# Kernel tuning notes

Hardware: AMD Instinct MI355X
Metric: run time of the kernel (lower is better)

## Reference

```python
import jax, jax.numpy as jnp
import numpy as np

D_MODEL = 768
STATE_N = 16
BATCH = 8
SEQ = 2048


def setup_inputs() -> dict:
    key = jax.random.key(0)
    ks = jax.random.split(key, 12)
    d, n = D_MODEL, STATE_N
    s = 0.02
    inp = {
        "x": jax.random.normal(ks[0], (BATCH, SEQ, d), dtype=jnp.float32),
        # A_log init as in module: log(arange(1..N)) repeated over d_model
        "A_log": jnp.log(jnp.tile(jnp.arange(1, n + 1, dtype=jnp.float32)[None, :], (d, 1))),
        "D_param": jnp.ones((d,), dtype=jnp.float32),
        "B_proj_w": jax.random.normal(ks[1], (n, d), dtype=jnp.float32) * s,
        "C_proj_w": jax.random.normal(ks[2], (n, d), dtype=jnp.float32) * s,
        "delta_w": jax.random.normal(ks[3], (d, d), dtype=jnp.float32) * s,
        "delta_b": jax.random.normal(ks[4], (d,), dtype=jnp.float32) * s,
        "in_w": jax.random.normal(ks[5], (2 * d, d), dtype=jnp.float32) * s,
        "in_b": jax.random.normal(ks[6], (2 * d,), dtype=jnp.float32) * s,
        "out_w": jax.random.normal(ks[7], (d, d), dtype=jnp.float32) * s,
        "out_b": jax.random.normal(ks[8], (d,), dtype=jnp.float32) * s,
        "conv_w": jax.random.normal(ks[9], (d, 1, 3), dtype=jnp.float32) * s,  # depthwise [D,1,K]
        "conv_b": jax.random.normal(ks[10], (d,), dtype=jnp.float32) * s,
    }
    return inp


def _forward(x, A_log, D_param, B_proj_w, C_proj_w, delta_w, delta_b,
             in_w, in_b, out_w, out_b, conv_w, conv_b):
    A = -jnp.exp(A_log)  # [D, N]
    xz = jnp.einsum("bld,ed->ble", x, in_w) + in_b  # [B, L, 2D]
    x_in, z = jnp.split(xz, 2, axis=-1)
    # depthwise conv1d, padding=1, groups=D (cross-correlation, same as torch)
    x_c = jax.lax.conv_general_dilated(
        jnp.transpose(x_in, (0, 2, 1)), conv_w,
        window_strides=(1,), padding=((1, 1),),
        feature_group_count=x.shape[-1],
        dimension_numbers=("NCH", "OIH", "NCH"))
    x_conv = jnp.transpose(x_c, (0, 2, 1)) + conv_b  # [B, L, D]
    x_conv = jax.nn.silu(x_conv)
    delta = jax.nn.softplus(jnp.einsum("bld,ed->ble", x_conv, delta_w) + delta_b)  # [B,L,D]
    B_sel = jnp.einsum("bld,nd->bln", x_conv, B_proj_w)  # [B, L, N]
    C_sel = jnp.einsum("bld,nd->bln", x_conv, C_proj_w)  # [B, L, N]

    Bsz, L, D = x.shape
    N = A.shape[1]

    def step(h, t_in):
        dt, b_t, c_t, x_t = t_in  # [B,D], [B,N], [B,N], [B,D]
        A_bar = jnp.exp(dt[:, :, None] * A[None, :, :])           # [B,D,N]
        h = A_bar * h + (dt[:, :, None] * b_t[:, None, :]) * x_t[:, :, None]
        y_t = jnp.sum(h * c_t[:, None, :], axis=-1)               # [B,D]
        return h, y_t

    xs = (jnp.transpose(delta, (1, 0, 2)), jnp.transpose(B_sel, (1, 0, 2)),
          jnp.transpose(C_sel, (1, 0, 2)), jnp.transpose(x_conv, (1, 0, 2)))
    h0 = jnp.zeros((Bsz, D, N), dtype=x.dtype)
    _, ys = jax.lax.scan(step, h0, xs)
    y = jnp.transpose(ys, (1, 0, 2))  # [B, L, D]

    y = y + x_conv * D_param[None, None, :]
    y = y * jax.nn.silu(z)
    return jnp.einsum("bld,ed->ble", y, out_w) + out_b


def reference(x, A_log, D_param, B_proj_w, C_proj_w, delta_w, delta_b,
              in_w, in_b, out_w, out_b, conv_w, conv_b):
    return _forward(x, A_log, D_param, B_proj_w, C_proj_w, delta_w, delta_b,
                    in_w, in_b, out_w, out_b, conv_w, conv_b)
```

## Files before the change

kernel.cpp:

```cpp
#include <hip/hip_runtime.h>
#include <hip/hip_bf16.h>

#define D_MODEL 768
#define SEQL    2048
#define BATCH   8
#define NSTATE  16
#define NCHUNK  32
#define TCHUNK  64

typedef __attribute__((ext_vector_type(8))) short short8;
typedef __attribute__((ext_vector_type(4))) float f32x4;

typedef const __attribute__((address_space(1))) unsigned int gas1_t;
typedef __attribute__((address_space(3))) unsigned int las3_t;

__device__ __forceinline__ void gload_lds16(const void* g, void* l) {
  __builtin_amdgcn_global_load_lds((gas1_t*)g, (las3_t*)l, 16, 0, 0);
}

__global__ __launch_bounds__(256) void prep_all(
    const float* __restrict__ x, const float* __restrict__ in_w,
    const float* __restrict__ delta_w, const float* __restrict__ Bp,
    const float* __restrict__ Cp, const float* __restrict__ out_w,
    const float* __restrict__ A_log,
    __hip_bfloat16* __restrict__ xb, __hip_bfloat16* __restrict__ w_in,
    __hip_bfloat16* __restrict__ w_dbc, __hip_bfloat16* __restrict__ w_out,
    float* __restrict__ A2) {
  int i = blockIdx.x * 256 + threadIdx.x;
  if (i < 3145728) {
    int j = i * 4;
    float4 v = *(const float4*)(x + j);
    xb[j + 0] = __float2bfloat16(v.x);
    xb[j + 1] = __float2bfloat16(v.y);
    xb[j + 2] = __float2bfloat16(v.z);
    xb[j + 3] = __float2bfloat16(v.w);
    return;
  }
  i -= 3145728;
  if (i < 1536 * 768) { w_in[i] = __float2bfloat16(in_w[i]); return; }
  i -= 1536 * 768;
  if (i < 896 * 768) {
    int row = i / 768, col = i - row * 768;
    float v;
    if (row < 768)      v = delta_w[row * 768 + col];
    else if (row < 784) v = Bp[(row - 768) * 768 + col];
    else if (row < 800) v = Cp[(row - 784) * 768 + col];
    else                v = 0.f;
    w_dbc[i] = __float2bfloat16(v);
    return;
  }
  i -= 896 * 768;
  if (i < 768 * 768) { w_out[i] = __float2bfloat16(out_w[i]); return; }
  i -= 768 * 768;
  A2[i] = -expf(A_log[i]) * 1.44269504088896f;
}

template <int MODE>
__global__ __launch_bounds__(256, 2) void gemm128(
    const __hip_bfloat16* __restrict__ Amat, const __hip_bfloat16* __restrict__ Bw,
    const float* __restrict__ bias, void* __restrict__ out0,
    void* __restrict__ out1, void* __restrict__ out2,
    const int K, const int gxn) {
  __shared__ char lds[65536];
  const int tid  = threadIdx.x;
  const int lane = tid & 63, wave = tid >> 6;
  const int wr = wave >> 1, wc = wave & 1;

  const int nwg = gridDim.x, id = blockIdx.x;
  const int swz = (id & 7) * (nwg >> 3) + (id >> 3);
  const int tm = swz / gxn, tn = swz - tm * gxn;
  const int rowA0 = tm * 128, rowB0 = tn * 128;

  const int srow = tid >> 3;
  const int scol = ((((tid & 7) << 4) ^ ((srow & 7) << 4)) >> 1);
  const __hip_bfloat16* gA = Amat + (size_t)(rowA0 + srow) * K + scol;
  const __hip_bfloat16* gB = Bw   + (size_t)(rowB0 + srow) * K + scol;
  const int ldst = tid << 4;

  const int frow = lane & 15, fq = lane >> 4;
  const int fswz = (frow & 7) << 4;
  const int pc0 = (fq << 4) ^ fswz;
  const int pc1 = (64 | (fq << 4)) ^ fswz;
  const int aro = (wr * 64 + frow) << 7;
  const int bro = (wc * 64 + frow) << 7;

  f32x4 acc[4][4];
#pragma unroll
  for (int m = 0; m < 4; ++m)
#pragma unroll
    for (int n = 0; n < 4; ++n) acc[m][n] = (f32x4){0.f, 0.f, 0.f, 0.f};

#define SA(buf) (lds + ((buf) << 15))
#define SB(buf) (lds + ((buf) << 15) + 16384)
#define STAGE(buf, kt)                                                          \
  {                                                                             \
    const __hip_bfloat16* spA = gA + (size_t)(kt) * 64;                         \
    const __hip_bfloat16* spB = gB + (size_t)(kt) * 64;                         \
    char* dA = SA(buf) + ldst;                                                  \
    char* dB = SB(buf) + ldst;                                                  \
    _Pragma("unroll") for (int ss = 0; ss < 4; ++ss)                            \
        gload_lds16(spA + (size_t)(ss * 32) * K, dA + ss * 4096);               \
    _Pragma("unroll") for (int ss = 0; ss < 4; ++ss)                            \
        gload_lds16(spB + (size_t)(ss * 32) * K, dB + ss * 4096);               \
  }

  short8 a[4][2], b[2][2];
#define LOADA(sAp)                                                              \
  {                                                                             \
    _Pragma("unroll") for (int m = 0; m < 4; ++m) {                             \
      const char* p = (sAp) + aro + ((m * 16) << 7);                            \
      a[m][0] = *(const short8*)(p + pc0);                                      \
      a[m][1] = *(const short8*)(p + pc1);                                      \
    }                                                                           \
  }
#define LOADB(sBp, nh)                                                          \
  {                                                                             \
    _Pragma("unroll") for (int n = 0; n < 2; ++n) {                             \
      const char* p = (sBp) + bro + ((((nh)*2 + n) * 16) << 7);                 \
      b[n][0] = *(const short8*)(p + pc0);                                      \
      b[n][1] = *(const short8*)(p + pc1);                                      \
    }                                                                           \
  }
#define MMA(nh)                                                                 \
  {                                                                             \
    __builtin_amdgcn_s_setprio(1);                                              \
    _Pragma("unroll") for (int m = 0; m < 4; ++m)                               \
    _Pragma("unroll") for (int n = 0; n < 2; ++n)                               \
    _Pragma("unroll") for (int ks = 0; ks < 2; ++ks)                            \
        acc[m][(nh)*2 + n] = __builtin_amdgcn_mfma_f32_16x16x32_bf16(           \
            a[m][ks], b[n][ks], acc[m][(nh)*2 + n], 0, 0, 0);                   \
    __builtin_amdgcn_s_setprio(0);                                              \
  }

  STAGE(0, 0);
  asm volatile("s_waitcnt vmcnt(0)" ::: "memory");
  __builtin_amdgcn_s_barrier();

  const int NT = K >> 6;
  for (int kt = 0; kt < NT; ++kt) {
    const int cur = kt & 1, nxt = cur ^ 1;
    const bool st = (kt + 1 < NT);
    LOADA(SA(cur));
    LOADB(SB(cur), 0);
    if (st) STAGE(nxt, kt + 1);
    __builtin_amdgcn_s_barrier();
    MMA(0);
    __builtin_amdgcn_s_barrier();
    LOADB(SB(cur), 1);
    __builtin_amdgcn_s_barrier();
    MMA(1);
    asm volatile("s_waitcnt vmcnt(0)" ::: "memory");
    __builtin_amdgcn_s_barrier();
  }

#pragma unroll
  for (int m = 0; m < 4; ++m) {
    const int grow0 = rowA0 + wr * 64 + m * 16 + fq * 4;
#pragma unroll
    for (int n = 0; n < 4; ++n) {
      const int gcol = rowB0 + wc * 64 + n * 16 + frow;
#pragma unroll
      for (int i = 0; i < 4; ++i) {
        const size_t grow = grow0 + i;
        float v = acc[m][n][i];
        if (MODE == 0) {
          v += bias[gcol];
          if (gcol < 768)
            ((__hip_bfloat16*)out0)[grow * 768 + gcol] = __float2bfloat16(v);
          else
            ((__hip_bfloat16*)out1)[grow * 768 + gcol - 768] = __float2bfloat16(v);
        } else if (MODE == 1) {
          if (gcol < 768) {
            v += bias[gcol];
            float sp = (v > 20.f) ? v : log1pf(expf(v));
            ((__hip_bfloat16*)out0)[grow * 768 + gcol] = __float2bfloat16(sp);
          } else if (gcol < 784) {
            ((float*)out1)[grow * 16 + (gcol - 768)] = v;
          } else if (gcol < 800) {
            ((float*)out2)[grow * 16 + (gcol - 784)] = v;
          }
        } else {
          ((float*)out0)[grow * 768 + gcol] = v + bias[gcol];
        }
      }
    }
  }
#undef SA
#undef SB
#undef STAGE
#undef LOADA
#undef LOADB
#undef MMA
}

__global__ __launch_bounds__(256) void conv_silu(
    const __hip_bfloat16* __restrict__ xin, const float* __restrict__ conv_w,
    const float* __restrict__ conv_b, __hip_bfloat16* __restrict__ xc) {
  const int idx = blockIdx.x * 256 + threadIdx.x;
  const int d = idx % 768;
  const int t = (idx / 768) % SEQL;
  const float w0 = conv_w[d * 3], w1 = conv_w[d * 3 + 1], w2 = conv_w[d * 3 + 2];
  float acc = conv_b[d];
  float xm = (t > 0)        ? __bfloat162float(xin[idx - 768]) : 0.f;
  float x0 = __bfloat162float(xin[idx]);
  float xp = (t < SEQL - 1) ? __bfloat162float(xin[idx + 768]) : 0.f;
  acc += w0 * xm + w1 * x0 + w2 * xp;
  const float sig = 1.f / (1.f + __expf(-acc));
  xc[idx] = __float2bfloat16(acc * sig);
}

__global__ __launch_bounds__(256) void scan_pass1(
    const __hip_bfloat16* __restrict__ delta, const __hip_bfloat16* __restrict__ xconv,
    const float* __restrict__ Bsel, const float* __restrict__ A2,
    float* __restrict__ sumdt, float* __restrict__ Sbuf) {
  const int d = blockIdx.x * 256 + threadIdx.x;
  const int b = blockIdx.y, c = blockIdx.z;
  __shared__ float sB[TCHUNK * 16];
  ((float4*)sB)[threadIdx.x] =
      ((const float4*)(Bsel + ((size_t)b * SEQL + c * TCHUNK) * 16))[threadIdx.x];
  __syncthreads();

  float a2[16];
#pragma unroll
  for (int n = 0; n < 16; ++n) a2[n] = A2[d * 16 + n];
  float h[16] = {};
  float sdt = 0.f;
  const size_t base = ((size_t)b * SEQL + c * TCHUNK) * 768 + d;
  for (int t = 0; t < TCHUNK; ++t) {
    const float dt = __bfloat162float(delta[base + (size_t)t * 768]);
    const float x = __bfloat162float(xconv[base + (size_t)t * 768]);
    sdt += dt;
    const float dtx = dt * x;
    const float* Br = &sB[t * 16];
#pragma unroll
    for (int n = 0; n < 16; ++n) {
      const float a = exp2f(dt * a2[n]);
      h[n] = fmaf(a, h[n], dtx * Br[n]);
    }
  }
  sumdt[((size_t)b * NCHUNK + c) * 768 + d] = sdt;
#pragma unroll
  for (int n = 0; n < 16; ++n)
    Sbuf[(((size_t)b * NCHUNK + c) * 16 + n) * 768 + d] = h[n];
}

__global__ __launch_bounds__(256) void scan_carry(
    const float* __restrict__ sumdt, const float* __restrict__ Sbuf,
    const float* __restrict__ A2, float* __restrict__ Hin) {
  const int idx = blockIdx.x * 256 + threadIdx.x;
  const int d = idx % 768;
  const int n = (idx / 768) & 15;
  const int b = idx / (768 * 16);
  const float a2 = A2[d * 16 + n];
  float h = 0.f;
  for (int c = 0; c < NCHUNK; ++c) {
    const size_t hb = (((size_t)(b * NCHUNK + c)) * 16 + n) * 768 + d;
    Hin[hb] = h;
    const float sd = sumdt[(b * NCHUNK + c) * 768 + d];
    h = fmaf(exp2f(sd * a2), h, Sbuf[hb]);
  }
}

__global__ __launch_bounds__(256) void scan_pass3(
    const __hip_bfloat16* __restrict__ delta, const __hip_bfloat16* __restrict__ xconv,
    const __hip_bfloat16* __restrict__ zb, const float* __restrict__ Bsel,
    const float* __restrict__ Csel, const float* __restrict__ A2,
    const float* __restrict__ Hin, const float* __restrict__ Dp,
    __hip_bfloat16* __restrict__ yg) {
  const int d = blockIdx.x * 256 + threadIdx.x;
  const int b = blockIdx.y, c = blockIdx.z;
  __shared__ float sB[TCHUNK * 16], sC[TCHUNK * 16];
  {
    const size_t off = ((size_t)b * SEQL + c * TCHUNK) * 16;
    ((float4*)sB)[threadIdx.x] = ((const float4*)(Bsel + off))[threadIdx.x];
    ((float4*)sC)[threadIdx.x] = ((const float4*)(Csel + off))[threadIdx.x];
  }
  __syncthreads();

  float a2[16];
#pragma unroll
  for (int n = 0; n < 16; ++n) a2[n] = A2[d * 16 + n];
  float h[16];
  {
    const size_t hb = ((size_t)b * NCHUNK + c) * 16 * 768 + d;
#pragma unroll
    for (int n = 0; n < 16; ++n) h[n] = Hin[hb + (size_t)n * 768];
  }
  const float Dpd = Dp[d];
  const size_t base = ((size_t)b * SEQL + c * TCHUNK) * 768 + d;
  for (int t = 0; t < TCHUNK; ++t) {
    const float dt = __bfloat162float(delta[base + (size_t)t * 768]);
    const float x = __bfloat162float(xconv[base + (size_t)t * 768]);
    const float dtx = dt * x;
    const float* Br = &sB[t * 16];
    const float* Cr = &sC[t * 16];
    float y = 0.f;
#pragma unroll
    for (int n = 0; n < 16; ++n) {
      const float a = exp2f(dt * a2[n]);
      h[n] = fmaf(a, h[n], dtx * Br[n]);
      y = fmaf(h[n], Cr[n], y);
    }
    const float z = __bfloat162float(zb[base + (size_t)t * 768]);
    const float sig = 1.f / (1.f + __expf(-z));
    const float out = (y + x * Dpd) * (z * sig);
    yg[base + (size_t)t * 768] = __float2bfloat16(out);
  }
}

extern "C" void kernel_launch(void* const* d_in, const int* in_sizes, int n_in,
                              void* d_out, int out_size, void* d_ws, size_t ws_size,
                              hipStream_t stream) {
  const float* x       = (const float*)d_in[0];
  const float* A_log   = (const float*)d_in[1];
  const float* D_param = (const float*)d_in[2];
  const float* B_proj  = (const float*)d_in[3];
  const float* C_proj  = (const float*)d_in[4];
  const float* delta_w = (const float*)d_in[5];
  const float* delta_b = (const float*)d_in[6];
  const float* in_w    = (const float*)d_in[7];
  const float* in_b    = (const float*)d_in[8];
  const float* out_w   = (const float*)d_in[9];
  const float* out_b   = (const float*)d_in[10];
  const float* conv_w  = (const float*)d_in[11];
  const float* conv_b  = (const float*)d_in[12];

  char* ws = (char*)d_ws;
  __hip_bfloat16* xb       = (__hip_bfloat16*)(ws + 0);
  __hip_bfloat16* w_in_b   = (__hip_bfloat16*)(ws + 25165824);
  __hip_bfloat16* w_dbc_b  = (__hip_bfloat16*)(ws + 27525120);
  __hip_bfloat16* w_out_b  = (__hip_bfloat16*)(ws + 28901376);
  float*          A2       = (float*)(ws + 30081024);
  __hip_bfloat16* xin_b    = (__hip_bfloat16*)(ws + 30130176);
  __hip_bfloat16* z_b      = (__hip_bfloat16*)(ws + 55296000);
  __hip_bfloat16* xconv_b  = (__hip_bfloat16*)(ws + 80461824);
  __hip_bfloat16* delta_bf = (__hip_bfloat16*)(ws + 105627648);
  float*          Bsel     = (float*)(ws + 130793472);
  float*          Csel     = (float*)(ws + 131842048);
  float*          sumdt    = (float*)(ws + 132890624);
  float*          Sbuf     = (float*)(ws + 133677056);
  float*          Hin      = (float*)(ws + 146259968);
  __hip_bfloat16* yg       = xb;

  const int BLD = BATCH * SEQL * D_MODEL;

  prep_all<<<21936, 256, 0, stream>>>(x, in_w, delta_w, B_proj, C_proj, out_w, A_log,
                                      xb, w_in_b, w_dbc_b, w_out_b, A2);
  gemm128<0><<<1536, 256, 0, stream>>>(xb, w_in_b, in_b, xin_b, z_b, nullptr, 768, 12);
  conv_silu<<<BLD / 256, 256, 0, stream>>>(xin_b, conv_w, conv_b, xconv_b);
  gemm128<1><<<896, 256, 0, stream>>>(xconv_b, w_dbc_b, delta_b, delta_bf, Bsel, Csel, 768, 7);
  scan_pass1<<<dim3(3, BATCH, NCHUNK), 256, 0, stream>>>(delta_bf, xconv_b, Bsel, A2, sumdt, Sbuf);
  scan_carry<<<384, 256, 0, stream>>>(sumdt, Sbuf, A2, Hin);
  scan_pass3<<<dim3(3, BATCH, NCHUNK), 256, 0, stream>>>(delta_bf, xconv_b, z_b, Bsel, Csel, A2,
                                                         Hin, D_param, yg);
  gemm128<2><<<768, 256, 0, stream>>>(yg, w_out_b, out_b, (float*)d_out, nullptr, nullptr, 768, 6);
}
```

Measured before the change: 383.9 us.

## Replace 128x128 GEMM with 256x256 tiled 8-wave kernel and interleaved staging

The GEMM kernel moves from 128x128 tiles with 4 waves to 256x256 tiles with 8 waves and 128KB of LDS. Global-to-LDS staging is split into quarter-tile pieces and interleaved with the four MMA phases using partial vmcnt waits. K is fixed at compile time. The delta/B/C weight matrix is padded to 1024 rows and the workspace offsets are shifted to match. The larger tiles should raise data reuse per byte loaded, but they cut the grid to 192-384 blocks, which risks poor CU utilisation. 128KB of LDS per block also likely keeps occupancy to one block per CU.

```diff
diff --git a/kernel.cpp b/kernel.cpp
--- a/kernel.cpp
+++ b/kernel.cpp
@@ -39,7 +39,7 @@
   i -= 3145728;
   if (i < 1536 * 768) { w_in[i] = __float2bfloat16(in_w[i]); return; }
   i -= 1536 * 768;
-  if (i < 896 * 768) {
+  if (i < 1024 * 768) {
     int row = i / 768, col = i - row * 768;
     float v;
     if (row < 768)      v = delta_w[row * 768 + col];
@@ -49,32 +49,32 @@
     w_dbc[i] = __float2bfloat16(v);
     return;
   }
-  i -= 896 * 768;
+  i -= 1024 * 768;
   if (i < 768 * 768) { w_out[i] = __float2bfloat16(out_w[i]); return; }
   i -= 768 * 768;
   A2[i] = -expf(A_log[i]) * 1.44269504088896f;
 }
 
 template <int MODE>
-__global__ __launch_bounds__(256, 2) void gemm128(
+__global__ __launch_bounds__(512, 2) void gemm256(
     const __hip_bfloat16* __restrict__ Amat, const __hip_bfloat16* __restrict__ Bw,
     const float* __restrict__ bias, void* __restrict__ out0,
-    void* __restrict__ out1, void* __restrict__ out2,
-    const int K, const int gxn) {
-  __shared__ char lds[65536];
+    void* __restrict__ out1, void* __restrict__ out2, const int gxn) {
+  constexpr int K = 768;
+  __shared__ char lds[131072];
   const int tid  = threadIdx.x;
   const int lane = tid & 63, wave = tid >> 6;
-  const int wr = wave >> 1, wc = wave & 1;
+  const int wr = wave >> 2, wc = wave & 3;
 
   const int nwg = gridDim.x, id = blockIdx.x;
   const int swz = (id & 7) * (nwg >> 3) + (id >> 3);
   const int tm = swz / gxn, tn = swz - tm * gxn;
-  const int rowA0 = tm * 128, rowB0 = tn * 128;
-
-  const int srow = tid >> 3;
-  const int scol = ((((tid & 7) << 4) ^ ((srow & 7) << 4)) >> 1);
-  const __hip_bfloat16* gA = Amat + (size_t)(rowA0 + srow) * K + scol;
-  const __hip_bfloat16* gB = Bw   + (size_t)(rowB0 + srow) * K + scol;
+  const int rowA0 = tm * 256, rowB0 = tn * 256;
+
+  const int srow0 = tid >> 3;
+  const int scol  = (((tid & 7) ^ (srow0 & 7)) << 3);
+  const __hip_bfloat16* gA = Amat + (size_t)(rowA0 + srow0) * K + scol;
+  const __hip_bfloat16* gB = Bw   + (size_t)(rowB0 + srow0) * K + scol;
   const int ldst = tid << 4;
 
   const int frow = lane & 15, fq = lane >> 4;
@@ -82,115 +82,155 @@
   const int pc0 = (fq << 4) ^ fswz;
   const int pc1 = (64 | (fq << 4)) ^ fswz;
   const int aro = (wr * 64 + frow) << 7;
-  const int bro = (wc * 64 + frow) << 7;
-
-  f32x4 acc[4][4];
-#pragma unroll
-  for (int m = 0; m < 4; ++m)
-#pragma unroll
-    for (int n = 0; n < 4; ++n) acc[m][n] = (f32x4){0.f, 0.f, 0.f, 0.f};
-
-#define SA(buf) (lds + ((buf) << 15))
-#define SB(buf) (lds + ((buf) << 15) + 16384)
-#define STAGE(buf, kt)                                                          \
-  {                                                                             \
-    const __hip_bfloat16* spA = gA + (size_t)(kt) * 64;                         \
-    const __hip_bfloat16* spB = gB + (size_t)(kt) * 64;                         \
-    char* dA = SA(buf) + ldst;                                                  \
-    char* dB = SB(buf) + ldst;                                                  \
-    _Pragma("unroll") for (int ss = 0; ss < 4; ++ss)                            \
-        gload_lds16(spA + (size_t)(ss * 32) * K, dA + ss * 4096);               \
-    _Pragma("unroll") for (int ss = 0; ss < 4; ++ss)                            \
-        gload_lds16(spB + (size_t)(ss * 32) * K, dB + ss * 4096);               \
+  const int bro = (wc * 32 + frow) << 7;
+
+  f32x4 acc[2][2][4][2];
+#pragma unroll
+  for (int mh = 0; mh < 2; ++mh)
+#pragma unroll
+    for (int nh = 0; nh < 2; ++nh)
+#pragma unroll
+      for (int m = 0; m < 4; ++m)
+#pragma unroll
+        for (int n = 0; n < 2; ++n) acc[mh][nh][m][n] = (f32x4){0.f, 0.f, 0.f, 0.f};
+
+#define STAGE_AH(d, h, kt)                                                      \
+  {                                                                             \
+    const __hip_bfloat16* s0 = gA + (size_t)((h)*128) * K + (kt)*64;            \
+    char* d0 = lds + ((d) << 16) + ((h) << 14) + ldst;                          \
+    gload_lds16(s0, d0);                                                        \
+    gload_lds16(s0 + (size_t)64 * K, d0 + 8192);                                \
+  }
+#define STAGE_BH(d, h, kt)                                                      \
+  {                                                                             \
+    const __hip_bfloat16* s0 = gB + (size_t)((h)*128) * K + (kt)*64;            \
+    char* d0 = lds + ((d) << 16) + 32768 + ((h) << 14) + ldst;                  \
+    gload_lds16(s0, d0);                                                        \
+    gload_lds16(s0 + (size_t)64 * K, d0 + 8192);                                \
   }
 
   short8 a[4][2], b[2][2];
-#define LOADA(sAp)                                                              \
-  {                                                                             \
+#define LOADA(d, mh)                                                            \
+  {                                                                             \
+    const char* base = lds + ((d) << 16) + ((mh) << 14) + aro;                  \
     _Pragma("unroll") for (int m = 0; m < 4; ++m) {                             \
-      const char* p = (sAp) + aro + ((m * 16) << 7);                            \
+      const char* p = base + ((m * 16) << 7);                                   \
       a[m][0] = *(const short8*)(p + pc0);                                      \
       a[m][1] = *(const short8*)(p + pc1);                                      \
     }                                                                           \
   }
-#define LOADB(sBp, nh)                                                          \
-  {                                                                             \
+#define LOADB(d, nh)                                                            \
+  {                                                                             \
+    const char* base = lds + ((d) << 16) + 32768 + ((nh) << 14) + bro;          \
     _Pragma("unroll") for (int n = 0; n < 2; ++n) {                             \
-      const char* p = (sBp) + bro + ((((nh)*2 + n) * 16) << 7);                 \
+      const char* p = base + ((n * 16) << 7);                                   \
       b[n][0] = *(const short8*)(p + pc0);                                      \
       b[n][1] = *(const short8*)(p + pc1);                                      \
     }                                                                           \
   }
-#define MMA(nh)                                                                 \
+#define MMA(mh, nh)                                                             \
   {                                                                             \
     __builtin_amdgcn_s_setprio(1);                                              \
     _Pragma("unroll") for (int m = 0; m < 4; ++m)                               \
     _Pragma("unroll") for (int n = 0; n < 2; ++n)                               \
     _Pragma("unroll") for (int ks = 0; ks < 2; ++ks)                            \
-        acc[m][(nh)*2 + n] = __builtin_amdgcn_mfma_f32_16x16x32_bf16(           \
-            a[m][ks], b[n][ks], acc[m][(nh)*2 + n], 0, 0, 0);                   \
+        acc[mh][nh][m][n] = __builtin_amdgcn_mfma_f32_16x16x32_bf16(            \
+            a[m][ks], b[n][ks], acc[mh][nh][m][n], 0, 0, 0);                    \
     __builtin_amdgcn_s_setprio(0);                                              \
   }
-
-  STAGE(0, 0);
-  asm volatile("s_waitcnt vmcnt(0)" ::: "memory");
-  __builtin_amdgcn_s_barrier();
-
-  const int NT = K >> 6;
-  for (int kt = 0; kt < NT; ++kt) {
+#define VMW(n) asm volatile("s_waitcnt vmcnt(" #n ")" ::: "memory")
+
+  STAGE_AH(0, 0, 0);
+  STAGE_BH(0, 0, 0);
+  STAGE_BH(0, 1, 0);
+  STAGE_AH(0, 1, 0);
+
+  constexpr int NT = K / 64;
+  for (int kt = 0; kt < NT - 1; ++kt) {
     const int cur = kt & 1, nxt = cur ^ 1;
-    const bool st = (kt + 1 < NT);
-    LOADA(SA(cur));
-    LOADB(SB(cur), 0);
-    if (st) STAGE(nxt, kt + 1);
-    __builtin_amdgcn_s_barrier();
-    MMA(0);
-    __builtin_amdgcn_s_barrier();
-    LOADB(SB(cur), 1);
-    __builtin_amdgcn_s_barrier();
-    MMA(1);
-    asm volatile("s_waitcnt vmcnt(0)" ::: "memory");
-    __builtin_amdgcn_s_barrier();
-  }
-
-#pragma unroll
-  for (int m = 0; m < 4; ++m) {
-    const int grow0 = rowA0 + wr * 64 + m * 16 + fq * 4;
-#pragma unroll
-    for (int n = 0; n < 4; ++n) {
-      const int gcol = rowB0 + wc * 64 + n * 16 + frow;
-#pragma unroll
-      for (int i = 0; i < 4; ++i) {
-        const size_t grow = grow0 + i;
-        float v = acc[m][n][i];
-        if (MODE == 0) {
-          v += bias[gcol];
-          if (gcol < 768)
-            ((__hip_bfloat16*)out0)[grow * 768 + gcol] = __float2bfloat16(v);
-          else
-            ((__hip_bfloat16*)out1)[grow * 768 + gcol - 768] = __float2bfloat16(v);
-        } else if (MODE == 1) {
-          if (gcol < 768) {
-            v += bias[gcol];
-            float sp = (v > 20.f) ? v : log1pf(expf(v));
-            ((__hip_bfloat16*)out0)[grow * 768 + gcol] = __float2bfloat16(sp);
-          } else if (gcol < 784) {
-            ((float*)out1)[grow * 16 + (gcol - 768)] = v;
-          } else if (gcol < 800) {
-            ((float*)out2)[grow * 16 + (gcol - 784)] = v;
+    VMW(4);
+    __builtin_amdgcn_s_barrier();
+    LOADA(cur, 0);
+    LOADB(cur, 0);
+    STAGE_AH(nxt, 0, kt + 1);
+    MMA(0, 0);
+    VMW(4);
+    __builtin_amdgcn_s_barrier();
+    LOADB(cur, 1);
+    STAGE_BH(nxt, 0, kt + 1);
+    MMA(0, 1);
+    VMW(4);
+    __builtin_amdgcn_s_barrier();
+    LOADA(cur, 1);
+    STAGE_BH(nxt, 1, kt + 1);
+    MMA(1, 1);
+    __builtin_amdgcn_s_barrier();
+    LOADB(cur, 0);
+    STAGE_AH(nxt, 1, kt + 1);
+    MMA(1, 0);
+  }
+  {
+    const int cur = (NT - 1) & 1;
+    VMW(4);
+    __builtin_amdgcn_s_barrier();
+    LOADA(cur, 0);
+    LOADB(cur, 0);
+    MMA(0, 0);
+    VMW(2);
+    __builtin_amdgcn_s_barrier();
+    LOADB(cur, 1);
+    MMA(0, 1);
+    VMW(0);
+    __builtin_amdgcn_s_barrier();
+    LOADA(cur, 1);
+    MMA(1, 1);
+    __builtin_amdgcn_s_barrier();
+    LOADB(cur, 0);
+    MMA(1, 0);
+  }
+
+#pragma unroll
+  for (int mh = 0; mh < 2; ++mh)
+#pragma unroll
+    for (int nh = 0; nh < 2; ++nh)
+#pragma unroll
+      for (int m = 0; m < 4; ++m) {
+        const int grow0 = rowA0 + mh * 128 + wr * 64 + m * 16 + fq * 4;
+#pragma unroll
+        for (int n = 0; n < 2; ++n) {
+          const int gcol = rowB0 + nh * 128 + wc * 32 + n * 16 + frow;
+#pragma unroll
+          for (int i = 0; i < 4; ++i) {
+            const size_t grow = grow0 + i;
+            float v = acc[mh][nh][m][n][i];
+            if (MODE == 0) {
+              v += bias[gcol];
+              if (gcol < 768)
+                ((__hip_bfloat16*)out0)[grow * 768 + gcol] = __float2bfloat16(v);
+              else
+                ((__hip_bfloat16*)out1)[grow * 768 + gcol - 768] = __float2bfloat16(v);
+            } else if (MODE == 1) {
+              if (gcol < 768) {
+                v += bias[gcol];
+                float sp = (v > 20.f) ? v : log1pf(expf(v));
+                ((__hip_bfloat16*)out0)[grow * 768 + gcol] = __float2bfloat16(sp);
+              } else if (gcol < 784) {
+                ((float*)out1)[grow * 16 + (gcol - 768)] = v;
+              } else if (gcol < 800) {
+                ((float*)out2)[grow * 16 + (gcol - 784)] = v;
+              }
+            } else {
+              ((float*)out0)[grow * 768 + gcol] = v + bias[gcol];
+            }
           }
-        } else {
-          ((float*)out0)[grow * 768 + gcol] = v + bias[gcol];
         }
       }
-    }
-  }
-#undef SA
-#undef SB
-#undef STAGE
+#undef STAGE_AH
+#undef STAGE_BH
 #undef LOADA
 #undef LOADB
 #undef MMA
+#undef VMW
 }
 
 __global__ __launch_bounds__(256) void conv_silu(
@@ -329,29 +369,29 @@
   __hip_bfloat16* xb       = (__hip_bfloat16*)(ws + 0);
   __hip_bfloat16* w_in_b   = (__hip_bfloat16*)(ws + 25165824);
   __hip_bfloat16* w_dbc_b  = (__hip_bfloat16*)(ws + 27525120);
-  __hip_bfloat16* w_out_b  = (__hip_bfloat16*)(ws + 28901376);
-  float*          A2       = (float*)(ws + 30081024);
-  __hip_bfloat16* xin_b    = (__hip_bfloat16*)(ws + 30130176);
-  __hip_bfloat16* z_b      = (__hip_bfloat16*)(ws + 55296000);
-  __hip_bfloat16* xconv_b  = (__hip_bfloat16*)(ws + 80461824);
-  __hip_bfloat16* delta_bf = (__hip_bfloat16*)(ws + 105627648);
-  float*          Bsel     = (float*)(ws + 130793472);
-  float*          Csel     = (float*)(ws + 131842048);
-  float*          sumdt    = (float*)(ws + 132890624);
-  float*          Sbuf     = (float*)(ws + 133677056);
-  float*          Hin      = (float*)(ws + 146259968);
+  __hip_bfloat16* w_out_b  = (__hip_bfloat16*)(ws + 29097984);
+  float*          A2       = (float*)(ws + 30277632);
+  __hip_bfloat16* xin_b    = (__hip_bfloat16*)(ws + 30326784);
+  __hip_bfloat16* z_b      = (__hip_bfloat16*)(ws + 55492608);
+  __hip_bfloat16* xconv_b  = (__hip_bfloat16*)(ws + 80658432);
+  __hip_bfloat16* delta_bf = (__hip_bfloat16*)(ws + 105824256);
+  float*          Bsel     = (float*)(ws + 130990080);
+  float*          Csel     = (float*)(ws + 132038656);
+  float*          sumdt    = (float*)(ws + 133087232);
+  float*          Sbuf     = (float*)(ws + 133873664);
+  float*          Hin      = (float*)(ws + 146456576);
   __hip_bfloat16* yg       = xb;
 
   const int BLD = BATCH * SEQL * D_MODEL;
 
-  prep_all<<<21936, 256, 0, stream>>>(x, in_w, delta_w, B_proj, C_proj, out_w, A_log,
+  prep_all<<<22320, 256, 0, stream>>>(x, in_w, delta_w, B_proj, C_proj, out_w, A_log,
                                       xb, w_in_b, w_dbc_b, w_out_b, A2);
-  gemm128<0><<<1536, 256, 0, stream>>>(xb, w_in_b, in_b, xin_b, z_b, nullptr, 768, 12);
+  gemm256<0><<<384, 512, 0, stream>>>(xb, w_in_b, in_b, xin_b, z_b, nullptr, 6);
   conv_silu<<<BLD / 256, 256, 0, stream>>>(xin_b, conv_w, conv_b, xconv_b);
-  gemm128<1><<<896, 256, 0, stream>>>(xconv_b, w_dbc_b, delta_b, delta_bf, Bsel, Csel, 768, 7);
+  gemm256<1><<<256, 512, 0, stream>>>(xconv_b, w_dbc_b, delta_b, delta_bf, Bsel, Csel, 4);
   scan_pass1<<<dim3(3, BATCH, NCHUNK), 256, 0, stream>>>(delta_bf, xconv_b, Bsel, A2, sumdt, Sbuf);
   scan_carry<<<384, 256, 0, stream>>>(sumdt, Sbuf, A2, Hin);
   scan_pass3<<<dim3(3, BATCH, NCHUNK), 256, 0, stream>>>(delta_bf, xconv_b, z_b, Bsel, Csel, A2,
                                                          Hin, D_param, yg);
-  gemm128<2><<<768, 256, 0, stream>>>(yg, w_out_b, out_b, (float*)d_out, nullptr, nullptr, 768, 6);
-}
+  gemm256<2><<<192, 512, 0, stream>>>(yg, w_out_b, out_b, (float*)d_out, nullptr, nullptr, 3);
+}
```

New measurement: 363.8 us. -5.2%, faster.

## Triple-buffer GEMM with BK=32 pipeline and vectorize conv_silu by 8

Applied to the files above, without the earlier changes.

The GEMM moves from a double-buffered BK=64 loop with four barriers per step to a triple-buffered BK=32 loop that prefetches two stages ahead, with one barrier per step. K is now a compile-time constant, and a smaller LDS footprint allows three workgroups per CU. The depthwise conv+SiLU now handles 8 channels per thread using 16-byte loads and stores, and the scan kernels use a cheaper bit-shift bf16-to-float conversion. The trade-off is twice as many loop iterations, each with fewer MFMAs to hide latency, plus higher register pressure from the 3-wave occupancy bound.

```diff
diff --git a/kernel.cpp b/kernel.cpp
--- a/kernel.cpp
+++ b/kernel.cpp
@@ -16,6 +16,14 @@
 
 __device__ __forceinline__ void gload_lds16(const void* g, void* l) {
   __builtin_amdgcn_global_load_lds((gas1_t*)g, (las3_t*)l, 16, 0, 0);
+}
+
+__device__ __forceinline__ float b2f(short s) {
+  return __uint_as_float(((unsigned)(unsigned short)s) << 16);
+}
+__device__ __forceinline__ short f2b(float f) {
+  __hip_bfloat16 h = __float2bfloat16(f);
+  return *reinterpret_cast<short*>(&h);
 }
 
 __global__ __launch_bounds__(256) void prep_all(
@@ -56,12 +64,13 @@
 }
 
 template <int MODE>
-__global__ __launch_bounds__(256, 2) void gemm128(
+__global__ __launch_bounds__(256, 3) void gemm128tb(
     const __hip_bfloat16* __restrict__ Amat, const __hip_bfloat16* __restrict__ Bw,
     const float* __restrict__ bias, void* __restrict__ out0,
-    void* __restrict__ out1, void* __restrict__ out2,
-    const int K, const int gxn) {
-  __shared__ char lds[65536];
+    void* __restrict__ out1, void* __restrict__ out2, const int gxn) {
+  constexpr int K  = 768;
+  constexpr int KT = 24;
+  __shared__ char lds[49152];
   const int tid  = threadIdx.x;
   const int lane = tid & 63, wave = tid >> 6;
   const int wr = wave >> 1, wc = wave & 1;
@@ -71,18 +80,16 @@
   const int tm = swz / gxn, tn = swz - tm * gxn;
   const int rowA0 = tm * 128, rowB0 = tn * 128;
 
-  const int srow = tid >> 3;
-  const int scol = ((((tid & 7) << 4) ^ ((srow & 7) << 4)) >> 1);
+  const int srow = tid >> 2;
+  const int scol = (((tid & 3) ^ ((srow >> 1) & 3)) << 3);
   const __hip_bfloat16* gA = Amat + (size_t)(rowA0 + srow) * K + scol;
   const __hip_bfloat16* gB = Bw   + (size_t)(rowB0 + srow) * K + scol;
   const int ldst = tid << 4;
 
   const int frow = lane & 15, fq = lane >> 4;
-  const int fswz = (frow & 7) << 4;
-  const int pc0 = (fq << 4) ^ fswz;
-  const int pc1 = (64 | (fq << 4)) ^ fswz;
-  const int aro = (wr * 64 + frow) << 7;
-  const int bro = (wc * 64 + frow) << 7;
+  const int pc = (fq << 4) ^ (((frow >> 1) & 3) << 4);
+  const int aoff = ((wr * 64 + frow) << 6) + pc;
+  const int boff = ((wc * 64 + frow) << 6) + pc;
 
   f32x4 acc[4][4];
 #pragma unroll
@@ -90,67 +97,49 @@
 #pragma unroll
     for (int n = 0; n < 4; ++n) acc[m][n] = (f32x4){0.f, 0.f, 0.f, 0.f};
 
-#define SA(buf) (lds + ((buf) << 15))
-#define SB(buf) (lds + ((buf) << 15) + 16384)
 #define STAGE(buf, kt)                                                          \
   {                                                                             \
-    const __hip_bfloat16* spA = gA + (size_t)(kt) * 64;                         \
-    const __hip_bfloat16* spB = gB + (size_t)(kt) * 64;                         \
-    char* dA = SA(buf) + ldst;                                                  \
-    char* dB = SB(buf) + ldst;                                                  \
-    _Pragma("unroll") for (int ss = 0; ss < 4; ++ss)                            \
-        gload_lds16(spA + (size_t)(ss * 32) * K, dA + ss * 4096);               \
-    _Pragma("unroll") for (int ss = 0; ss < 4; ++ss)                            \
-        gload_lds16(spB + (size_t)(ss * 32) * K, dB + ss * 4096);               \
-  }
-
-  short8 a[4][2], b[2][2];
-#define LOADA(sAp)                                                              \
-  {                                                                             \
-    _Pragma("unroll") for (int m = 0; m < 4; ++m) {                             \
-      const char* p = (sAp) + aro + ((m * 16) << 7);                            \
-      a[m][0] = *(const short8*)(p + pc0);                                      \
-      a[m][1] = *(const short8*)(p + pc1);                                      \
-    }                                                                           \
-  }
-#define LOADB(sBp, nh)                                                          \
-  {                                                                             \
-    _Pragma("unroll") for (int n = 0; n < 2; ++n) {                             \
-      const char* p = (sBp) + bro + ((((nh)*2 + n) * 16) << 7);                 \
-      b[n][0] = *(const short8*)(p + pc0);                                      \
-      b[n][1] = *(const short8*)(p + pc1);                                      \
-    }                                                                           \
-  }
-#define MMA(nh)                                                                 \
-  {                                                                             \
-    __builtin_amdgcn_s_setprio(1);                                              \
-    _Pragma("unroll") for (int m = 0; m < 4; ++m)                               \
-    _Pragma("unroll") for (int n = 0; n < 2; ++n)                               \
-    _Pragma("unroll") for (int ks = 0; ks < 2; ++ks)                            \
-        acc[m][(nh)*2 + n] = __builtin_amdgcn_mfma_f32_16x16x32_bf16(           \
-            a[m][ks], b[n][ks], acc[m][(nh)*2 + n], 0, 0, 0);                   \
-    __builtin_amdgcn_s_setprio(0);                                              \
-  }
+    const __hip_bfloat16* sA = gA + (kt) * 32;                                  \
+    const __hip_bfloat16* sB = gB + (kt) * 32;                                  \
+    char* dA = lds + (buf) * 16384 + ldst;                                      \
+    char* dB = dA + 8192;                                                       \
+    gload_lds16(sA, dA);                                                        \
+    gload_lds16(sA + (size_t)64 * K, dA + 4096);                                \
+    gload_lds16(sB, dB);                                                        \
+    gload_lds16(sB + (size_t)64 * K, dB + 4096);                                \
+  }
+#define VMW(n) asm volatile("s_waitcnt vmcnt(" #n ")" ::: "memory")
+#define BAR    __builtin_amdgcn_s_barrier()
 
   STAGE(0, 0);
-  asm volatile("s_waitcnt vmcnt(0)" ::: "memory");
-  __builtin_amdgcn_s_barrier();
-
-  const int NT = K >> 6;
-  for (int kt = 0; kt < NT; ++kt) {
-    const int cur = kt & 1, nxt = cur ^ 1;
-    const bool st = (kt + 1 < NT);
-    LOADA(SA(cur));
-    LOADB(SB(cur), 0);
-    if (st) STAGE(nxt, kt + 1);
-    __builtin_amdgcn_s_barrier();
-    MMA(0);
-    __builtin_amdgcn_s_barrier();
-    LOADB(SB(cur), 1);
-    __builtin_amdgcn_s_barrier();
-    MMA(1);
-    asm volatile("s_waitcnt vmcnt(0)" ::: "memory");
-    __builtin_amdgcn_s_barrier();
+  STAGE(1, 1);
+  VMW(4);
+  BAR;
+
+  int bc = 0;
+  for (int kt = 0; kt < KT; ++kt) {
+    short8 a[4], b[4];
+    const char* ba = lds + bc * 16384;
+#pragma unroll
+    for (int m = 0; m < 4; ++m) a[m] = *(const short8*)(ba + aoff + m * 1024);
+#pragma unroll
+    for (int n = 0; n < 4; ++n) b[n] = *(const short8*)(ba + 8192 + boff + n * 1024);
+    const bool st = (kt + 2 < KT);
+    if (st) {
+      const int b2 = bc + 2 >= 3 ? bc - 1 : bc + 2;
+      STAGE(b2, kt + 2);
+    }
+    __builtin_amdgcn_s_setprio(1);
+#pragma unroll
+    for (int m = 0; m < 4; ++m)
+#pragma unroll
+      for (int n = 0; n < 4; ++n)
+        acc[m][n] = __builtin_amdgcn_mfma_f32_16x16x32_bf16(a[m], b[n], acc[m][n], 0, 0, 0);
+    __builtin_amdgcn_s_setprio(0);
+    if (st)                VMW(4);
+    else if (kt + 2 == KT) VMW(0);
+    BAR;
+    bc = bc + 1 >= 3 ? 0 : bc + 1;
   }
 
 #pragma unroll
@@ -185,28 +174,45 @@
       }
     }
   }
-#undef SA
-#undef SB
 #undef STAGE
-#undef LOADA
-#undef LOADB
-#undef MMA
-}
-
-__global__ __launch_bounds__(256) void conv_silu(
+#undef VMW
+#undef BAR
+}
+
+__global__ __launch_bounds__(256) void conv_silu8(
     const __hip_bfloat16* __restrict__ xin, const float* __restrict__ conv_w,
     const float* __restrict__ conv_b, __hip_bfloat16* __restrict__ xc) {
   const int idx = blockIdx.x * 256 + threadIdx.x;
-  const int d = idx % 768;
-  const int t = (idx / 768) % SEQL;
-  const float w0 = conv_w[d * 3], w1 = conv_w[d * 3 + 1], w2 = conv_w[d * 3 + 2];
-  float acc = conv_b[d];
-  float xm = (t > 0)        ? __bfloat162float(xin[idx - 768]) : 0.f;
-  float x0 = __bfloat162float(xin[idx]);
-  float xp = (t < SEQL - 1) ? __bfloat162float(xin[idx + 768]) : 0.f;
-  acc += w0 * xm + w1 * x0 + w2 * xp;
-  const float sig = 1.f / (1.f + __expf(-acc));
-  xc[idx] = __float2bfloat16(acc * sig);
+  const int d8 = (idx % 96) * 8;
+  const int t  = (idx / 96) % SEQL;
+  const size_t base = (size_t)idx * 8;
+
+  short8 x0 = *(const short8*)(xin + base);
+  short8 xm = {}, xp = {};
+  if (t > 0)        xm = *(const short8*)(xin + base - 768);
+  if (t < SEQL - 1) xp = *(const short8*)(xin + base + 768);
+
+  const float4* cw4 = (const float4*)(conv_w + d8 * 3);
+  float4 cw[6];
+#pragma unroll
+  for (int q = 0; q < 6; ++q) cw[q] = cw4[q];
+  float4 cb0 = *(const float4*)(conv_b + d8);
+  float4 cb1 = *(const float4*)(conv_b + d8 + 4);
+  const float* cwf = (const float*)cw;
+  const float* cbf0 = (const float*)&cb0;
+  const float* cbf1 = (const float*)&cb1;
+
+  short8 r;
+#pragma unroll
+  for (int e = 0; e < 8; ++e) {
+    float acc = (e < 4) ? cbf0[e] : cbf1[e - 4];
+    acc = fmaf(cwf[e * 3 + 0], b2f(xm[e]), acc);
+    acc = fmaf(cwf[e * 3 + 1], b2f(x0[e]), acc);
+    acc = fmaf(cwf[e * 3 + 2], b2f(xp[e]), acc);
+    const float sig = 1.f / (1.f + __expf(-acc));
+    r[e] = f2b(acc * sig);
+  }
+  *(short8*)(xc + base) = r;
 }
 
 __global__ __launch_bounds__(256) void scan_pass1(
@@ -227,8 +233,8 @@
   float sdt = 0.f;
   const size_t base = ((size_t)b * SEQL + c * TCHUNK) * 768 + d;
   for (int t = 0; t < TCHUNK; ++t) {
-    const float dt = __bfloat162float(delta[base + (size_t)t * 768]);
-    const float x = __bfloat162float(xconv[base + (size_t)t * 768]);
+    const float dt = b2f(((const short*)delta)[base + (size_t)t * 768]);
+    const float x = b2f(((const short*)xconv)[base + (size_t)t * 768]);
     sdt += dt;
     const float dtx = dt * x;
     const float* Br = &sB[t * 16];
@@ -289,8 +295,8 @@
   const float Dpd = Dp[d];
   const size_t base = ((size_t)b * SEQL + c * TCHUNK) * 768 + d;
   for (int t = 0; t < TCHUNK; ++t) {
-    const float dt = __bfloat162float(delta[base + (size_t)t * 768]);
-    const float x = __bfloat162float(xconv[base + (size_t)t * 768]);
+    const float dt = b2f(((const short*)delta)[base + (size_t)t * 768]);
+    const float x = b2f(((const short*)xconv)[base + (size_t)t * 768]);
     const float dtx = dt * x;
     const float* Br = &sB[t * 16];
     const float* Cr = &sC[t * 16];
@@ -301,7 +307,7 @@
       h[n] = fmaf(a, h[n], dtx * Br[n]);
       y = fmaf(h[n], Cr[n], y);
     }
-    const float z = __bfloat162float(zb[base + (size_t)t * 768]);
+    const float z = b2f(((const short*)zb)[base + (size_t)t * 768]);
     const float sig = 1.f / (1.f + __expf(-z));
     const float out = (y + x * Dpd) * (z * sig);
     yg[base + (size_t)t * 768] = __float2bfloat16(out);
@@ -346,12 +352,12 @@
 
   prep_all<<<21936, 256, 0, stream>>>(x, in_w, delta_w, B_proj, C_proj, out_w, A_log,
                                       xb, w_in_b, w_dbc_b, w_out_b, A2);
-  gemm128<0><<<1536, 256, 0, stream>>>(xb, w_in_b, in_b, xin_b, z_b, nullptr, 768, 12);
-  conv_silu<<<BLD / 256, 256, 0, stream>>>(xin_b, conv_w, conv_b, xconv_b);
-  gemm128<1><<<896, 256, 0, stream>>>(xconv_b, w_dbc_b, delta_b, delta_bf, Bsel, Csel, 768, 7);
+  gemm128tb<0><<<1536, 256, 0, stream>>>(xb, w_in_b, in_b, xin_b, z_b, nullptr, 12);
+  conv_silu8<<<BLD / 8 / 256, 256, 0, stream>>>(xin_b, conv_w, conv_b, xconv_b);
+  gemm128tb<1><<<896, 256, 0, stream>>>(xconv_b, w_dbc_b, delta_b, delta_bf, Bsel, Csel, 7);
   scan_pass1<<<dim3(3, BATCH, NCHUNK), 256, 0, stream>>>(delta_bf, xconv_b, Bsel, A2, sumdt, Sbuf);
   scan_carry<<<384, 256, 0, stream>>>(sumdt, Sbuf, A2, Hin);
   scan_pass3<<<dim3(3, BATCH, NCHUNK), 256, 0, stream>>>(delta_bf, xconv_b, z_b, Bsel, Csel, A2,
                                                          Hin, D_param, yg);
-  gemm128<2><<<768, 256, 0, stream>>>(yg, w_out_b, out_b, (float*)d_out, nullptr, nullptr, 768, 6);
-}
+  gemm128tb<2><<<768, 256, 0, stream>>>(yg, w_out_b, out_b, (float*)d_out, nullptr, nullptr, 6);
+}
```

Result: faster. 347.0 us (-9.6%).
